# Kernel optimization log

Hardware: AMD Instinct MI355X
Metric: run time of the kernel (lower is better)

## Reference

```python
import jax, jax.numpy as jnp
import numpy as np

N = 50000
E = 800000
IN_DIM = 128
HID = 64
HEADS = 4
OUT = 64


def _bn(x, g, b, eps=1e-5):
    # BatchNorm1d with batch statistics (biased var), as in train-mode normalization
    mu = x.mean(0)
    var = ((x - mu) ** 2).mean(0)
    return (x - mu) * jax.lax.rsqrt(var + eps) * g + b


def _gat(x, W, a_src, a_dst, bias, src, dst, heads, dim, concat):
    # PyG GATConv: h = xW; e_ij = LeakyReLU(a_src.h_j + a_dst.h_i); softmax over incoming edges of i
    n = x.shape[0]
    h = (x @ W).reshape(n, heads, dim)            # [N,H,D]
    es = (h * a_src).sum(-1)                      # [N,H]
    ed = (h * a_dst).sum(-1)                      # [N,H]
    e = jax.nn.leaky_relu(es[src] + ed[dst], 0.2)  # [E,H]
    emax = jax.ops.segment_max(e, dst, num_segments=n)
    w = jnp.exp(e - emax[dst])
    denom = jax.ops.segment_sum(w, dst, num_segments=n)
    alpha = w / (denom[dst] + 1e-16)              # [E,H]
    out = jax.ops.segment_sum(h[src] * alpha[:, :, None], dst, num_segments=n)  # [N,H,D]
    out = out.reshape(n, heads * dim) if concat else out.mean(axis=1)
    return out + bias


def _gcn(x, W, bias, src, dst):
    # PyG GCNConv with self-loops (already appended): D^{-1/2} A D^{-1/2} x W
    n = x.shape[0]
    h = x @ W
    deg = jax.ops.segment_sum(jnp.ones(src.shape[0], h.dtype), dst, num_segments=n)
    dinv = jax.lax.rsqrt(jnp.maximum(deg, 1e-12))
    norm = dinv[src] * dinv[dst]                  # [E]
    return jax.ops.segment_sum(h[src] * norm[:, None], dst, num_segments=n) + bias


def setup_inputs() -> dict:
    key = jax.random.key(0)
    ks = jax.random.split(key, 16)
    s = 0.1
    inp = {
        "x": jax.random.normal(ks[0], (N, IN_DIM), jnp.float32),
        "edge_index": jax.random.randint(ks[1], (2, E), 0, N, jnp.int64 if jax.config.jax_enable_x64 else jnp.int32),
        "edge_attr": jax.random.normal(ks[2], (E,), jnp.float32),
        # GAT layer 1
        "W1": jax.random.normal(ks[3], (IN_DIM, HEADS * HID), jnp.float32) * s,
        "att_src1": jax.random.normal(ks[4], (HEADS, HID), jnp.float32) * s,
        "att_dst1": jax.random.normal(ks[5], (HEADS, HID), jnp.float32) * s,
        "b1": jnp.zeros((HEADS * HID,), jnp.float32),
        "g1": jnp.ones((HEADS * HID,), jnp.float32),
        "beta1": jnp.zeros((HEADS * HID,), jnp.float32),
        # GCN
        "Wg": jax.random.normal(ks[6], (HEADS * HID, HID), jnp.float32) * s,
        "bg": jnp.zeros((HID,), jnp.float32),
        "g2": jnp.ones((HID,), jnp.float32),
        "beta2": jnp.zeros((HID,), jnp.float32),
        # GAT layer 2 (heads=1, concat=False)
        "W2": jax.random.normal(ks[7], (HID, OUT), jnp.float32) * s,
        "att_src2": jax.random.normal(ks[8], (1, OUT), jnp.float32) * s,
        "att_dst2": jax.random.normal(ks[9], (1, OUT), jnp.float32) * s,
        "b2": jnp.zeros((OUT,), jnp.float32),
        "g3": jnp.ones((OUT,), jnp.float32),
        "beta3": jnp.zeros((OUT,), jnp.float32),
        # projector
        "Wp1": jax.random.normal(ks[10], (OUT, 128), jnp.float32) * s,
        "bp1": jnp.zeros((128,), jnp.float32),
        "Wp2": jax.random.normal(ks[11], (128, 64), jnp.float32) * s,
        "bp2": jnp.zeros((64,), jnp.float32),
    }
    return inp


def reference(x, edge_index, edge_attr, W1, att_src1, att_dst1, b1, g1, beta1,
              Wg, bg, g2, beta2, W2, att_src2, att_dst2, b2, g3, beta3,
              Wp1, bp1, Wp2, bp2):
    # edge_attr is ignored by GATConv when edge_dim is None (PyG behavior)
    loop = jnp.arange(N, dtype=edge_index.dtype)
    src = jnp.concatenate([edge_index[0], loop])  # self-loops appended
    dst = jnp.concatenate([edge_index[1], loop])
    h = _gat(x, W1, att_src1, att_dst1, b1, src, dst, HEADS, HID, True)
    h = jax.nn.elu(_bn(h, g1, beta1))
    h = _gcn(h, Wg, bg, src, dst)
    h = jax.nn.relu(_bn(h, g2, beta2))
    h = _gat(h, W2, att_src2, att_dst2, b2, src, dst, 1, OUT, False)
    h = jax.nn.elu(_bn(h, g3, beta3))
    return jax.nn.relu(h @ Wp1 + bp1) @ Wp2 + bp2
```

## Files before the change

kernel.cpp:

```cpp
#include <hip/hip_runtime.h>
#include <math.h>

#define NN 50000
#define EE 800000
#define E2 850000
#define SCB 196
#define GXL 391

typedef __attribute__((ext_vector_type(8))) short short8;
typedef __attribute__((ext_vector_type(8))) unsigned short ushort8v;
typedef __attribute__((ext_vector_type(4))) float float4v;

__device__ __forceinline__ float bf2f(unsigned short u) {
  return __uint_as_float(((unsigned int)u) << 16);
}
__device__ __forceinline__ unsigned short f2bf(float f) {
  unsigned int x = __float_as_uint(f);
  unsigned int r = (x + 0x7fffu + ((x >> 16) & 1u)) >> 16;
  return (unsigned short)r;
}

__device__ __forceinline__ float leaky(float x) { return x > 0.f ? x : 0.2f * x; }

__device__ __forceinline__ int edge_src(const int* ei, int e) {
  return (e < EE) ? ei[e] : (e - EE);
}
__device__ __forceinline__ int edge_dst(const int* ei, int e) {
  return (e < EE) ? ei[EE + e] : (e - EE);
}

__global__ void k_deg(const int* __restrict__ ei, int* __restrict__ deg) {
  int e = blockIdx.x * blockDim.x + threadIdx.x;
  if (e < E2) atomicAdd(&deg[edge_dst(ei, e)], 1);
}

__global__ __launch_bounds__(256) void k_scan1(const int* __restrict__ deg,
                                               int* __restrict__ partial) {
  __shared__ int sd[256];
  int i = blockIdx.x * 256 + threadIdx.x;
  sd[threadIdx.x] = (i < NN) ? deg[i] : 0;
  __syncthreads();
  for (int off = 128; off > 0; off >>= 1) {
    if (threadIdx.x < off) sd[threadIdx.x] += sd[threadIdx.x + off];
    __syncthreads();
  }
  if (threadIdx.x == 0) partial[blockIdx.x] = sd[0];
}

__global__ __launch_bounds__(256) void k_scan3(const int* __restrict__ deg,
                                               const int* __restrict__ partial,
                                               int* __restrict__ rowptr,
                                               int* __restrict__ cnt,
                                               float* __restrict__ dinv) {
  __shared__ int sp[256];
  __shared__ int sd[256];
  int t = threadIdx.x;
  sp[t] = (t < SCB) ? partial[t] : 0;
  __syncthreads();
  for (int off = 1; off < 256; off <<= 1) {
    int v = (t >= off) ? sp[t - off] : 0;
    __syncthreads();
    sp[t] += v;
    __syncthreads();
  }
  int base = (blockIdx.x == 0) ? 0 : sp[blockIdx.x - 1];
  int i = blockIdx.x * 256 + t;
  int v = (i < NN) ? deg[i] : 0;
  sd[t] = v;
  __syncthreads();
  for (int off = 1; off < 256; off <<= 1) {
    int u = (t >= off) ? sd[t - off] : 0;
    __syncthreads();
    sd[t] += u;
    __syncthreads();
  }
  if (i < NN) {
    int excl = base + sd[t] - v;
    rowptr[i] = excl;
    cnt[i] = excl;
    dinv[i] = rsqrtf((float)v);
  }
  if (i == 0) rowptr[NN] = E2;
}

__global__ void k_fill(const int* __restrict__ ei, int* __restrict__ cnt,
                       int* __restrict__ csr) {
  int e = blockIdx.x * blockDim.x + threadIdx.x;
  if (e >= E2) return;
  int d = edge_dst(ei, e);
  int s = edge_src(ei, e);
  int pos = atomicAdd(&cnt[d], 1);
  csr[pos] = s;
}

__global__ __launch_bounds__(256) void k_gemm1(
    const float* __restrict__ A, const float* __restrict__ B,
    unsigned short* __restrict__ Cbf,
    const float* __restrict__ attSrc, const float* __restrict__ attDst,
    float* __restrict__ esOut, float* __restrict__ edOut, int M) {
  __shared__ unsigned short BT[64][136];
  int t = threadIdx.x;
  int lane = t & 63;
  int wv = t >> 6;
  int cl = lane & 15;
  int kg = lane >> 4;
  int rowBase = blockIdx.x * 128;

  short8 afr[2][4];
  int grA0 = rowBase + wv * 32 + cl;
#pragma unroll
  for (int rt = 0; rt < 2; ++rt) {
    int gr = grA0 + rt * 16;
#pragma unroll
    for (int ks = 0; ks < 4; ++ks) {
      int k0 = ks * 32 + kg * 8;
      if (gr < M) {
        float4 f0 = *(const float4*)&A[(size_t)gr * 128 + k0];
        float4 f1 = *(const float4*)&A[(size_t)gr * 128 + k0 + 4];
        afr[rt][ks][0] = (short)f2bf(f0.x); afr[rt][ks][1] = (short)f2bf(f0.y);
        afr[rt][ks][2] = (short)f2bf(f0.z); afr[rt][ks][3] = (short)f2bf(f0.w);
        afr[rt][ks][4] = (short)f2bf(f1.x); afr[rt][ks][5] = (short)f2bf(f1.y);
        afr[rt][ks][6] = (short)f2bf(f1.z); afr[rt][ks][7] = (short)f2bf(f1.w);
      } else {
#pragma unroll
        for (int j = 0; j < 8; ++j) afr[rt][ks][j] = 0;
      }
    }
  }

  for (int cg = 0; cg < 4; ++cg) {
    int colBase = cg * 64;
    {
      int c = t & 63;
      for (int k = t >> 6; k < 128; k += 4)
        BT[c][k] = f2bf(B[(size_t)k * 256 + colBase + c]);
    }
    __syncthreads();

    float4v acc[2][4];
#pragma unroll
    for (int rt = 0; rt < 2; ++rt)
#pragma unroll
      for (int ct = 0; ct < 4; ++ct) acc[rt][ct] = (float4v){0.f, 0.f, 0.f, 0.f};

#pragma unroll
    for (int ks = 0; ks < 4; ++ks) {
      int k0 = ks * 32 + kg * 8;
      short8 bfr[4];
#pragma unroll
      for (int ct = 0; ct < 4; ++ct)
        bfr[ct] = *(const short8*)&BT[ct * 16 + cl][k0];
#pragma unroll
      for (int rt = 0; rt < 2; ++rt)
#pragma unroll
        for (int ct = 0; ct < 4; ++ct)
          acc[rt][ct] = __builtin_amdgcn_mfma_f32_16x16x32_bf16(
              afr[rt][ks], bfr[ct], acc[rt][ct], 0, 0, 0);
    }

    float as4[4], ad4[4];
#pragma unroll
    for (int ct = 0; ct < 4; ++ct) {
      int gc = colBase + ct * 16 + cl;
      as4[ct] = attSrc[gc];
      ad4[ct] = attDst[gc];
    }
#pragma unroll
    for (int rt = 0; rt < 2; ++rt) {
      float pes[4] = {0.f, 0.f, 0.f, 0.f};
      float ped[4] = {0.f, 0.f, 0.f, 0.f};
#pragma unroll
      for (int reg = 0; reg < 4; ++reg) {
        int gr = rowBase + wv * 32 + rt * 16 + kg * 4 + reg;
        bool ok = gr < M;
#pragma unroll
        for (int ct = 0; ct < 4; ++ct) {
          float v = acc[rt][ct][reg];
          int gc = colBase + ct * 16 + cl;
          if (ok) Cbf[(size_t)gr * 256 + gc] = f2bf(v);
          pes[reg] = fmaf(v, as4[ct], pes[reg]);
          ped[reg] = fmaf(v, ad4[ct], ped[reg]);
        }
      }
#pragma unroll
      for (int reg = 0; reg < 4; ++reg) {
#pragma unroll
        for (int off = 8; off > 0; off >>= 1) {
          pes[reg] += __shfl_xor(pes[reg], off);
          ped[reg] += __shfl_xor(ped[reg], off);
        }
      }
      if (cl == 0) {
#pragma unroll
        for (int reg = 0; reg < 4; ++reg) {
          int gr = rowBase + wv * 32 + rt * 16 + kg * 4 + reg;
          if (gr < M) {
            esOut[gr * 4 + cg] = pes[reg];
            edOut[gr * 4 + cg] = ped[reg];
          }
        }
      }
    }
    __syncthreads();
  }
}

template <int K, int ATTMODE, int INACT, bool ABF, bool USEBN>
__global__ __launch_bounds__(256) void k_gemm_mfma(
    const float* __restrict__ A, const unsigned short* __restrict__ Abf,
    const float* __restrict__ B, const float* __restrict__ biasOut,
    const float* __restrict__ bnst, const float* __restrict__ bng,
    const float* __restrict__ bnb, int outAct,
    float* __restrict__ Cf, unsigned short* __restrict__ Cbf,
    const float* __restrict__ rowScale,
    const float* __restrict__ attSrc, const float* __restrict__ attDst,
    float* __restrict__ esOut, float* __restrict__ edOut,
    int M, int NC) {
  __shared__ unsigned short BT[64][K + 8];
  __shared__ float sSc[256], sSh[256];
  int t = threadIdx.x;
  int lane = t & 63;
  int wv = t >> 6;
  int cl = lane & 15;
  int kg = lane >> 4;
  int rowBase = blockIdx.x * 128;
  int colBase = blockIdx.y * 64;

  if (USEBN) {
    int c = t;
    if (c < K) {
      float sum = 0.f, sq = 0.f;
      for (int cp = 0; cp < 32; ++cp) {
        sum += bnst[cp * 2 * K + c];
        sq += bnst[cp * 2 * K + K + c];
      }
      const float invN = 1.0f / (float)NN;
      float mu = sum * invN;
      float var = sq * invN - mu * mu;
      float rs = rsqrtf(var + 1e-5f);
      float sc = rs * bng[c];
      sSc[c] = sc;
      sSh[c] = fmaf(-mu, sc, bnb[c]);
    }
  }
  {
    int c = t & 63;
    for (int k = t >> 6; k < K; k += 4)
      BT[c][k] = f2bf(B[(size_t)k * NC + colBase + c]);
  }
  __syncthreads();

  float4v acc[2][4];
#pragma unroll
  for (int rt = 0; rt < 2; ++rt)
#pragma unroll
    for (int ct = 0; ct < 4; ++ct) acc[rt][ct] = (float4v){0.f, 0.f, 0.f, 0.f};

  int grA0 = rowBase + wv * 32 + cl;
  int grA1 = grA0 + 16;

#pragma unroll
  for (int kc = 0; kc < K; kc += 32) {
    int k0 = kc + kg * 8;
    short8 afr[2];
#pragma unroll
    for (int rt = 0; rt < 2; ++rt) {
      int gr = rt ? grA1 : grA0;
      float v[8];
      if (gr < M) {
        if (ABF) {
          ushort4 u0 = *(const ushort4*)&Abf[(size_t)gr * K + k0];
          ushort4 u1 = *(const ushort4*)&Abf[(size_t)gr * K + k0 + 4];
          v[0] = bf2f(u0.x); v[1] = bf2f(u0.y); v[2] = bf2f(u0.z); v[3] = bf2f(u0.w);
          v[4] = bf2f(u1.x); v[5] = bf2f(u1.y); v[6] = bf2f(u1.z); v[7] = bf2f(u1.w);
        } else {
          float4 f0 = *(const float4*)&A[(size_t)gr * K + k0];
          float4 f1 = *(const float4*)&A[(size_t)gr * K + k0 + 4];
          v[0] = f0.x; v[1] = f0.y; v[2] = f0.z; v[3] = f0.w;
          v[4] = f1.x; v[5] = f1.y; v[6] = f1.z; v[7] = f1.w;
        }
      } else {
#pragma unroll
        for (int i = 0; i < 8; ++i) v[i] = 0.f;
      }
#pragma unroll
      for (int i = 0; i < 8; ++i) {
        float x = v[i];
        if (USEBN) x = fmaf(x, sSc[k0 + i], sSh[k0 + i]);
        if (INACT == 1) x = fmaxf(x, 0.f);
        else if (INACT == 2) x = (x > 0.f) ? x : expm1f(x);
        afr[rt][i] = (short)f2bf(x);
      }
    }
    short8 bfr[4];
#pragma unroll
    for (int ct = 0; ct < 4; ++ct)
      bfr[ct] = *(const short8*)&BT[ct * 16 + cl][k0];
#pragma unroll
    for (int rt = 0; rt < 2; ++rt)
#pragma unroll
      for (int ct = 0; ct < 4; ++ct)
        acc[rt][ct] = __builtin_amdgcn_mfma_f32_16x16x32_bf16(
            afr[rt], bfr[ct], acc[rt][ct], 0, 0, 0);
  }

  float bb[4], as4[4], ad4[4];
#pragma unroll
  for (int ct = 0; ct < 4; ++ct) {
    int gc = colBase + ct * 16 + cl;
    bb[ct] = biasOut ? biasOut[gc] : 0.f;
    if (ATTMODE) {
      as4[ct] = attSrc[gc];
      ad4[ct] = attDst[gc];
    }
  }
#pragma unroll
  for (int rt = 0; rt < 2; ++rt) {
    float pes[4] = {0.f, 0.f, 0.f, 0.f};
    float ped[4] = {0.f, 0.f, 0.f, 0.f};
#pragma unroll
    for (int reg = 0; reg < 4; ++reg) {
      int gr = rowBase + wv * 32 + rt * 16 + kg * 4 + reg;
      bool ok = gr < M;
      float rs_ = 1.f;
      if (ok && Cbf && rowScale) rs_ = rowScale[gr];
#pragma unroll
      for (int ct = 0; ct < 4; ++ct) {
        float v = acc[rt][ct][reg] + bb[ct];
        if (outAct == 1) v = fmaxf(v, 0.f);
        int gc = colBase + ct * 16 + cl;
        if (ok) {
          if (Cf) Cf[(size_t)gr * NC + gc] = v;
          if (Cbf) Cbf[(size_t)gr * NC + gc] = f2bf(v * rs_);
        }
        if (ATTMODE) {
          pes[reg] = fmaf(v, as4[ct], pes[reg]);
          ped[reg] = fmaf(v, ad4[ct], ped[reg]);
        }
      }
    }
    if (ATTMODE) {
#pragma unroll
      for (int reg = 0; reg < 4; ++reg) {
#pragma unroll
        for (int off = 8; off > 0; off >>= 1) {
          pes[reg] += __shfl_xor(pes[reg], off);
          ped[reg] += __shfl_xor(ped[reg], off);
        }
      }
      if (cl == 0) {
#pragma unroll
        for (int reg = 0; reg < 4; ++reg) {
          int gr = rowBase + wv * 32 + rt * 16 + kg * 4 + reg;
          if (gr < M) {
            if (ATTMODE == 1) {
              esOut[gr * 4 + blockIdx.y] = pes[reg];
              edOut[gr * 4 + blockIdx.y] = ped[reg];
            } else {
              esOut[gr] = pes[reg];
              edOut[gr] = ped[reg];
            }
          }
        }
      }
    }
  }
}

__global__ __launch_bounds__(256) void k_soft1(const float* __restrict__ es,
                                               const float* __restrict__ ed,
                                               const int* __restrict__ rowptr,
                                               const int* __restrict__ csr,
                                               float* __restrict__ w1) {
  int node = blockIdx.x * 16 + (threadIdx.x >> 4);
  int sub = threadIdx.x & 15;
  int start = rowptr[node], end = rowptr[node + 1];
  float4 edv = *(const float4*)&ed[node * 4];
  float m0 = -1e30f, m1 = -1e30f, m2 = -1e30f, m3 = -1e30f;
  float s0 = 0.f, s1 = 0.f, s2 = 0.f, s3 = 0.f;
  for (int k = start + sub; k < end; k += 16) {
    int s = csr[k];
    float4 esv = *(const float4*)&es[s * 4];
    float e0 = leaky(esv.x + edv.x);
    float e1 = leaky(esv.y + edv.y);
    float e2 = leaky(esv.z + edv.z);
    float e3 = leaky(esv.w + edv.w);
    float mn;
    mn = fmaxf(m0, e0); s0 = s0 * __expf(m0 - mn) + __expf(e0 - mn); m0 = mn;
    mn = fmaxf(m1, e1); s1 = s1 * __expf(m1 - mn) + __expf(e1 - mn); m1 = mn;
    mn = fmaxf(m2, e2); s2 = s2 * __expf(m2 - mn) + __expf(e2 - mn); m2 = mn;
    mn = fmaxf(m3, e3); s3 = s3 * __expf(m3 - mn) + __expf(e3 - mn); m3 = mn;
  }
#pragma unroll
  for (int off = 1; off < 16; off <<= 1) {
    float mo, so, mn;
    mo = __shfl_xor(m0, off); so = __shfl_xor(s0, off);
    mn = fmaxf(m0, mo); s0 = s0 * __expf(m0 - mn) + so * __expf(mo - mn); m0 = mn;
    mo = __shfl_xor(m1, off); so = __shfl_xor(s1, off);
    mn = fmaxf(m1, mo); s1 = s1 * __expf(m1 - mn) + so * __expf(mo - mn); m1 = mn;
    mo = __shfl_xor(m2, off); so = __shfl_xor(s2, off);
    mn = fmaxf(m2, mo); s2 = s2 * __expf(m2 - mn) + so * __expf(mo - mn); m2 = mn;
    mo = __shfl_xor(m3, off); so = __shfl_xor(s3, off);
    mn = fmaxf(m3, mo); s3 = s3 * __expf(m3 - mn) + so * __expf(mo - mn); m3 = mn;
  }
  float i0 = 1.f / (s0 + 1e-16f);
  float i1 = 1.f / (s1 + 1e-16f);
  float i2 = 1.f / (s2 + 1e-16f);
  float i3 = 1.f / (s3 + 1e-16f);
  for (int k = start + sub; k < end; k += 16) {
    int s = csr[k];
    float4 esv = *(const float4*)&es[s * 4];
    w1[k]          = __expf(leaky(esv.x + edv.x) - m0) * i0;
    w1[E2 + k]     = __expf(leaky(esv.y + edv.y) - m1) * i1;
    w1[2 * E2 + k] = __expf(leaky(esv.z + edv.z) - m2) * i2;
    w1[3 * E2 + k] = __expf(leaky(esv.w + edv.w) - m3) * i3;
  }
}

__global__ __launch_bounds__(256) void k_soft2(const float* __restrict__ es,
                                               const float* __restrict__ ed,
                                               const int* __restrict__ rowptr,
                                               const int* __restrict__ csr,
                                               float* __restrict__ w2) {
  int node = blockIdx.x * 16 + (threadIdx.x >> 4);
  int sub = threadIdx.x & 15;
  int start = rowptr[node], end = rowptr[node + 1];
  float edi = ed[node];
  float m = -1e30f, ss = 0.f;
  for (int k = start + sub; k < end; k += 16) {
    float e = leaky(es[csr[k]] + edi);
    float mn = fmaxf(m, e);
    ss = ss * __expf(m - mn) + __expf(e - mn);
    m = mn;
  }
#pragma unroll
  for (int off = 1; off < 16; off <<= 1) {
    float mo = __shfl_xor(m, off);
    float so = __shfl_xor(ss, off);
    float mn = fmaxf(m, mo);
    ss = ss * __expf(m - mn) + so * __expf(mo - mn);
    m = mn;
  }
  float inv = 1.f / (ss + 1e-16f);
  for (int k = start + sub; k < end; k += 16) {
    float e = leaky(es[csr[k]] + edi);
    w2[k] = __expf(e - m) * inv;
  }
}

__global__ __launch_bounds__(256) void k_gat1(const unsigned short* __restrict__ h1b,
                                              const float* __restrict__ w1,
                                              const int* __restrict__ rowptr,
                                              const int* __restrict__ csr,
                                              const float* __restrict__ b1,
                                              unsigned short* __restrict__ outb,
                                              float* __restrict__ st) {
  __shared__ float smS[4][256];
  __shared__ float smQ[4][256];
  int wave = threadIdx.x >> 6;
  int lane = threadIdx.x & 63;
  int i = blockIdx.x * 4 + wave;
  int start = rowptr[i], end = rowptr[i + 1];
  int half = lane >> 5;
  int cl5 = lane & 31;
  int head = cl5 >> 3;
  int cOff = cl5 * 8;
  const float* wh = w1 + (size_t)head * E2;
  float acc[8];
#pragma unroll
  for (int j = 0; j < 8; ++j) acc[j] = 0.f;

  int k = start;
  for (; k + 4 <= end; k += 4) {
#pragma unroll
    for (int u = 0; u < 2; ++u) {
      int kk = k + u * 2 + half;
      int s = csr[kk];
      float wv = wh[kk];
      ushort8v hv = *(const ushort8v*)&h1b[(size_t)s * 256 + cOff];
#pragma unroll
      for (int j = 0; j < 8; ++j) acc[j] = fmaf(bf2f(hv[j]), wv, acc[j]);
    }
  }
  for (; k + 2 <= end; k += 2) {
    int kk = k + half;
    int s = csr[kk];
    float wv = wh[kk];
    ushort8v hv = *(const ushort8v*)&h1b[(size_t)s * 256 + cOff];
#pragma unroll
    for (int j = 0; j < 8; ++j) acc[j] = fmaf(bf2f(hv[j]), wv, acc[j]);
  }
  if (k < end) {
    int s = csr[k];
    float wv = (half == 0) ? wh[k] : 0.f;
    ushort8v hv = *(const ushort8v*)&h1b[(size_t)s * 256 + cOff];
#pragma unroll
    for (int j = 0; j < 8; ++j) acc[j] = fmaf(bf2f(hv[j]), wv, acc[j]);
  }
#pragma unroll
  for (int j = 0; j < 8; ++j) acc[j] += __shfl_xor(acc[j], 32);

  float4 b0 = *(const float4*)&b1[cOff];
  float4 b1v = *(const float4*)&b1[cOff + 4];
  float bb[8] = {b0.x, b0.y, b0.z, b0.w, b1v.x, b1v.y, b1v.z, b1v.w};
  if (half == 0) {
    float o[8];
    ushort8v u8;
#pragma unroll
    for (int j = 0; j < 8; ++j) {
      o[j] = acc[j] + bb[j];
      u8[j] = f2bf(o[j]);
    }
    *(ushort8v*)&outb[(size_t)i * 256 + cOff] = u8;
    float4 s0 = make_float4(o[0], o[1], o[2], o[3]);
    float4 s1 = make_float4(o[4], o[5], o[6], o[7]);
    *(float4*)&smS[wave][cOff] = s0;
    *(float4*)&smS[wave][cOff + 4] = s1;
    float4 q0 = make_float4(o[0]*o[0], o[1]*o[1], o[2]*o[2], o[3]*o[3]);
    float4 q1 = make_float4(o[4]*o[4], o[5]*o[5], o[6]*o[6], o[7]*o[7]);
    *(float4*)&smQ[wave][cOff] = q0;
    *(float4*)&smQ[wave][cOff + 4] = q1;
  }
  __syncthreads();
  int c = threadIdx.x;
  float s_ = 0.f, q_ = 0.f;
#pragma unroll
  for (int wv = 0; wv < 4; ++wv) { s_ += smS[wv][c]; q_ += smQ[wv][c]; }
  float* dst = st + (size_t)(blockIdx.x & 31) * 512;
  atomicAdd(&dst[c], s_);
  atomicAdd(&dst[256 + c], q_);
}

__global__ __launch_bounds__(256) void k_gcn(const unsigned short* __restrict__ hgb,
                                             const float* __restrict__ dinv,
                                             const int* __restrict__ rowptr,
                                             const int* __restrict__ csr,
                                             const float* __restrict__ bg,
                                             unsigned short* __restrict__ outb,
                                             float* __restrict__ st) {
  __shared__ float smS[4][64];
  __shared__ float smQ[4][64];
  int wave = threadIdx.x >> 6;
  int lane = threadIdx.x & 63;
  int i = blockIdx.x * 4 + wave;
  int start = rowptr[i], end = rowptr[i + 1];
  int grp = lane >> 3;
  int cOff = (lane & 7) * 8;
  float acc[8];
#pragma unroll
  for (int j = 0; j < 8; ++j) acc[j] = 0.f;

  int k = start;
  for (; k + 8 <= end; k += 8) {
    int s = csr[k + grp];
    ushort8v hv = *(const ushort8v*)&hgb[(size_t)s * 64 + cOff];
#pragma unroll
    for (int j = 0; j < 8; ++j) acc[j] += bf2f(hv[j]);
  }
  if (k < end) {
    int kk = k + grp;
    bool act = kk < end;
    int s = csr[act ? kk : start];
    float m_ = act ? 1.f : 0.f;
    ushort8v hv = *(const ushort8v*)&hgb[(size_t)s * 64 + cOff];
#pragma unroll
    for (int j = 0; j < 8; ++j) acc[j] = fmaf(bf2f(hv[j]), m_, acc[j]);
  }
#pragma unroll
  for (int off = 8; off <= 32; off <<= 1)
#pragma unroll
    for (int j = 0; j < 8; ++j) acc[j] += __shfl_xor(acc[j], off);

  if (lane < 8) {
    float di = dinv[i];
    float4 g0 = *(const float4*)&bg[cOff];
    float4 g1 = *(const float4*)&bg[cOff + 4];
    float bb[8] = {g0.x, g0.y, g0.z, g0.w, g1.x, g1.y, g1.z, g1.w};
    float o[8];
    ushort8v u8;
#pragma unroll
    for (int j = 0; j < 8; ++j) {
      o[j] = fmaf(acc[j], di, bb[j]);
      u8[j] = f2bf(o[j]);
      smS[wave][cOff + j] = o[j];
      smQ[wave][cOff + j] = o[j] * o[j];
    }
    *(ushort8v*)&outb[(size_t)i * 64 + cOff] = u8;
  }
  __syncthreads();
  if (threadIdx.x < 64) {
    int c = threadIdx.x;
    float s_ = 0.f, q_ = 0.f;
#pragma unroll
    for (int wv = 0; wv < 4; ++wv) { s_ += smS[wv][c]; q_ += smQ[wv][c]; }
    float* dst = st + (size_t)(blockIdx.x & 31) * 128;
    atomicAdd(&dst[c], s_);
    atomicAdd(&dst[64 + c], q_);
  }
}

__global__ __launch_bounds__(256) void k_gat2(const unsigned short* __restrict__ h2b,
                                              const float* __restrict__ w2,
                                              const int* __restrict__ rowptr,
                                              const int* __restrict__ csr,
                                              const float* __restrict__ b2,
                                              unsigned short* __restrict__ outb,
                                              float* __restrict__ st) {
  __shared__ float smS[4][64];
  __shared__ float smQ[4][64];
  int wave = threadIdx.x >> 6;
  int lane = threadIdx.x & 63;
  int i = blockIdx.x * 4 + wave;
  int start = rowptr[i], end = rowptr[i + 1];
  int grp = lane >> 3;
  int cOff = (lane & 7) * 8;
  float acc[8];
#pragma unroll
  for (int j = 0; j < 8; ++j) acc[j] = 0.f;

  int k = start;
  for (; k + 8 <= end; k += 8) {
    int kk = k + grp;
    int s = csr[kk];
    float wv = w2[kk];
    ushort8v hv = *(const ushort8v*)&h2b[(size_t)s * 64 + cOff];
#pragma unroll
    for (int j = 0; j < 8; ++j) acc[j] = fmaf(bf2f(hv[j]), wv, acc[j]);
  }
  if (k < end) {
    int kk = k + grp;
    bool act = kk < end;
    int s = csr[act ? kk : start];
    float wv = act ? w2[kk] : 0.f;
    ushort8v hv = *(const ushort8v*)&h2b[(size_t)s * 64 + cOff];
#pragma unroll
    for (int j = 0; j < 8; ++j) acc[j] = fmaf(bf2f(hv[j]), wv, acc[j]);
  }
#pragma unroll
  for (int off = 8; off <= 32; off <<= 1)
#pragma unroll
    for (int j = 0; j < 8; ++j) acc[j] += __shfl_xor(acc[j], off);

  if (lane < 8) {
    float4 g0 = *(const float4*)&b2[cOff];
    float4 g1 = *(const float4*)&b2[cOff + 4];
    float bb[8] = {g0.x, g0.y, g0.z, g0.w, g1.x, g1.y, g1.z, g1.w};
    float o[8];
    ushort8v u8;
#pragma unroll
    for (int j = 0; j < 8; ++j) {
      o[j] = acc[j] + bb[j];
      u8[j] = f2bf(o[j]);
      smS[wave][cOff + j] = o[j];
      smQ[wave][cOff + j] = o[j] * o[j];
    }
    *(ushort8v*)&outb[(size_t)i * 64 + cOff] = u8;
  }
  __syncthreads();
  if (threadIdx.x < 64) {
    int c = threadIdx.x;
    float s_ = 0.f, q_ = 0.f;
#pragma unroll
    for (int wv = 0; wv < 4; ++wv) { s_ += smS[wv][c]; q_ += smQ[wv][c]; }
    float* dst = st + (size_t)(blockIdx.x & 31) * 128;
    atomicAdd(&dst[c], s_);
    atomicAdd(&dst[64 + c], q_);
  }
}

extern "C" void kernel_launch(void* const* d_in, const int* in_sizes, int n_in,
                              void* d_out, int out_size, void* d_ws, size_t ws_size,
                              hipStream_t stream) {
  const float* x        = (const float*)d_in[0];
  const int*   ei       = (const int*)d_in[1];
  const float* W1       = (const float*)d_in[3];
  const float* att_src1 = (const float*)d_in[4];
  const float* att_dst1 = (const float*)d_in[5];
  const float* b1       = (const float*)d_in[6];
  const float* g1       = (const float*)d_in[7];
  const float* beta1    = (const float*)d_in[8];
  const float* Wg       = (const float*)d_in[9];
  const float* bg       = (const float*)d_in[10];
  const float* g2       = (const float*)d_in[11];
  const float* beta2    = (const float*)d_in[12];
  const float* W2       = (const float*)d_in[13];
  const float* att_src2 = (const float*)d_in[14];
  const float* att_dst2 = (const float*)d_in[15];
  const float* b2       = (const float*)d_in[16];
  const float* g3       = (const float*)d_in[17];
  const float* beta3    = (const float*)d_in[18];
  const float* Wp1      = (const float*)d_in[19];
  const float* bp1      = (const float*)d_in[20];
  const float* Wp2      = (const float*)d_in[21];
  const float* bp2      = (const float*)d_in[22];
  float* out = (float*)d_out;

  char* w = (char*)d_ws;
  unsigned short* bufBb  = (unsigned short*)(w + 0);
  unsigned short* bufDb  = (unsigned short*)(w + 0);
  unsigned short* h1b    = (unsigned short*)(w + 51200000);
  unsigned short* hiddenb= (unsigned short*)(w + 51200000);
  float*          w1     = (float*)(w + 76800000);
  float*          w2     = (float*)(w + 76800000);
  unsigned short* hgb    = (unsigned short*)(w + 90400000);
  unsigned short* bufCb  = (unsigned short*)(w + 96800000);
  unsigned short* h2b    = (unsigned short*)(w + 109600000);
  float*          es1    = (float*)(w + 116000000);
  float*          ed1    = (float*)(w + 116800000);
  float*          es2    = (float*)(w + 117600000);
  float*          ed2    = (float*)(w + 117800000);
  float*          dinv   = (float*)(w + 118000000);
  int*            deg    = (int*)(w + 118200000);
  int*            rowptr = (int*)(w + 118400000);
  int*            cnt    = (int*)(w + 118600064);
  int*            csr    = (int*)(w + 118800064);
  float*          st1    = (float*)(w + 122200064);
  float*          st2    = st1 + 32 * 512;
  float*          st3    = st2 + 32 * 128;
  int*            partial= (int*)(st3 + 32 * 128);

  hipMemsetAsync(deg, 0, NN * sizeof(int), stream);
  hipMemsetAsync(st1, 0, (32 * 512 + 32 * 128 + 32 * 128) * sizeof(float), stream);

  const int EB = (E2 + 255) / 256;
  const int WB = NN / 4;
  const int SB = NN / 16;

  k_deg<<<EB, 256, 0, stream>>>(ei, deg);
  k_scan1<<<SCB, 256, 0, stream>>>(deg, partial);
  k_scan3<<<SCB, 256, 0, stream>>>(deg, partial, rowptr, cnt, dinv);
  k_fill<<<EB, 256, 0, stream>>>(ei, cnt, csr);

  k_gemm1<<<GXL, 256, 0, stream>>>(x, W1, h1b, att_src1, att_dst1, es1, ed1, NN);
  k_soft1<<<SB, 256, 0, stream>>>(es1, ed1, rowptr, csr, w1);
  k_gat1<<<WB, 256, 0, stream>>>(h1b, w1, rowptr, csr, b1, bufBb, st1);

  k_gemm_mfma<256, 0, 2, true, true><<<dim3(GXL, 1), 256, 0, stream>>>(
      nullptr, bufBb, Wg, nullptr, st1, g1, beta1, 0,
      nullptr, hgb, dinv, nullptr, nullptr, nullptr, nullptr, NN, 64);
  k_gcn<<<WB, 256, 0, stream>>>(hgb, dinv, rowptr, csr, bg, bufCb, st2);

  k_gemm_mfma<64, 2, 1, true, true><<<dim3(GXL, 1), 256, 0, stream>>>(
      nullptr, bufCb, W2, nullptr, st2, g2, beta2, 0,
      nullptr, h2b, nullptr, att_src2, att_dst2, es2, ed2, NN, 64);
  k_soft2<<<SB, 256, 0, stream>>>(es2, ed2, rowptr, csr, w2);
  k_gat2<<<WB, 256, 0, stream>>>(h2b, w2, rowptr, csr, b2, bufDb, st3);

  k_gemm_mfma<64, 0, 2, true, true><<<dim3(GXL, 2), 256, 0, stream>>>(
      nullptr, bufDb, Wp1, bp1, st3, g3, beta3, 1,
      nullptr, hiddenb, nullptr, nullptr, nullptr, nullptr, nullptr, NN, 128);
  k_gemm_mfma<128, 0, 0, true, false><<<dim3(GXL, 1), 256, 0, stream>>>(
      nullptr, hiddenb, Wp2, bp2, nullptr, nullptr, nullptr, 0,
      out, nullptr, nullptr, nullptr, nullptr, nullptr, nullptr, NN, 64);
}
```

Measured before the change: 450.0 us.

## Fuse edge softmax into GAT aggregation kernels, dropping the attention weight buffers

Removes the separate k_soft1/k_soft2 kernels. Each GAT aggregation wave now computes the per-node online max and sum over incoming edges itself, then recomputes the normalized attention weight inline from es/ed while gathering neighbor features. This avoids writing and re-reading the E x 4 (and E x 1) float weight arrays and saves two launches. In exchange, es is gathered twice per edge and the exponentials are evaluated redundantly across the lanes that share a head.

```diff
diff --git a/kernel.cpp b/kernel.cpp
--- a/kernel.cpp
+++ b/kernel.cpp
@@ -367,18 +367,25 @@
   }
 }
 
-__global__ __launch_bounds__(256) void k_soft1(const float* __restrict__ es,
-                                               const float* __restrict__ ed,
-                                               const int* __restrict__ rowptr,
-                                               const int* __restrict__ csr,
-                                               float* __restrict__ w1) {
-  int node = blockIdx.x * 16 + (threadIdx.x >> 4);
-  int sub = threadIdx.x & 15;
-  int start = rowptr[node], end = rowptr[node + 1];
-  float4 edv = *(const float4*)&ed[node * 4];
+__global__ __launch_bounds__(256) void k_gat1(const unsigned short* __restrict__ h1b,
+                                              const float* __restrict__ es,
+                                              const float* __restrict__ ed,
+                                              const int* __restrict__ rowptr,
+                                              const int* __restrict__ csr,
+                                              const float* __restrict__ b1,
+                                              unsigned short* __restrict__ outb,
+                                              float* __restrict__ st) {
+  __shared__ float smS[4][256];
+  __shared__ float smQ[4][256];
+  int wave = threadIdx.x >> 6;
+  int lane = threadIdx.x & 63;
+  int i = blockIdx.x * 4 + wave;
+  int start = rowptr[i], end = rowptr[i + 1];
+  float4 edv = *(const float4*)&ed[i * 4];
+
   float m0 = -1e30f, m1 = -1e30f, m2 = -1e30f, m3 = -1e30f;
   float s0 = 0.f, s1 = 0.f, s2 = 0.f, s3 = 0.f;
-  for (int k = start + sub; k < end; k += 16) {
+  for (int k = start + lane; k < end; k += 64) {
     int s = csr[k];
     float4 esv = *(const float4*)&es[s * 4];
     float e0 = leaky(esv.x + edv.x);
@@ -392,7 +399,7 @@
     mn = fmaxf(m3, e3); s3 = s3 * __expf(m3 - mn) + __expf(e3 - mn); m3 = mn;
   }
 #pragma unroll
-  for (int off = 1; off < 16; off <<= 1) {
+  for (int off = 1; off < 64; off <<= 1) {
     float mo, so, mn;
     mo = __shfl_xor(m0, off); so = __shfl_xor(s0, off);
     mn = fmaxf(m0, mo); s0 = s0 * __expf(m0 - mn) + so * __expf(mo - mn); m0 = mn;
@@ -403,69 +410,16 @@
     mo = __shfl_xor(m3, off); so = __shfl_xor(s3, off);
     mn = fmaxf(m3, mo); s3 = s3 * __expf(m3 - mn) + so * __expf(mo - mn); m3 = mn;
   }
-  float i0 = 1.f / (s0 + 1e-16f);
-  float i1 = 1.f / (s1 + 1e-16f);
-  float i2 = 1.f / (s2 + 1e-16f);
-  float i3 = 1.f / (s3 + 1e-16f);
-  for (int k = start + sub; k < end; k += 16) {
-    int s = csr[k];
-    float4 esv = *(const float4*)&es[s * 4];
-    w1[k]          = __expf(leaky(esv.x + edv.x) - m0) * i0;
-    w1[E2 + k]     = __expf(leaky(esv.y + edv.y) - m1) * i1;
-    w1[2 * E2 + k] = __expf(leaky(esv.z + edv.z) - m2) * i2;
-    w1[3 * E2 + k] = __expf(leaky(esv.w + edv.w) - m3) * i3;
-  }
-}
-
-__global__ __launch_bounds__(256) void k_soft2(const float* __restrict__ es,
-                                               const float* __restrict__ ed,
-                                               const int* __restrict__ rowptr,
-                                               const int* __restrict__ csr,
-                                               float* __restrict__ w2) {
-  int node = blockIdx.x * 16 + (threadIdx.x >> 4);
-  int sub = threadIdx.x & 15;
-  int start = rowptr[node], end = rowptr[node + 1];
-  float edi = ed[node];
-  float m = -1e30f, ss = 0.f;
-  for (int k = start + sub; k < end; k += 16) {
-    float e = leaky(es[csr[k]] + edi);
-    float mn = fmaxf(m, e);
-    ss = ss * __expf(m - mn) + __expf(e - mn);
-    m = mn;
-  }
-#pragma unroll
-  for (int off = 1; off < 16; off <<= 1) {
-    float mo = __shfl_xor(m, off);
-    float so = __shfl_xor(ss, off);
-    float mn = fmaxf(m, mo);
-    ss = ss * __expf(m - mn) + so * __expf(mo - mn);
-    m = mn;
-  }
-  float inv = 1.f / (ss + 1e-16f);
-  for (int k = start + sub; k < end; k += 16) {
-    float e = leaky(es[csr[k]] + edi);
-    w2[k] = __expf(e - m) * inv;
-  }
-}
-
-__global__ __launch_bounds__(256) void k_gat1(const unsigned short* __restrict__ h1b,
-                                              const float* __restrict__ w1,
-                                              const int* __restrict__ rowptr,
-                                              const int* __restrict__ csr,
-                                              const float* __restrict__ b1,
-                                              unsigned short* __restrict__ outb,
-                                              float* __restrict__ st) {
-  __shared__ float smS[4][256];
-  __shared__ float smQ[4][256];
-  int wave = threadIdx.x >> 6;
-  int lane = threadIdx.x & 63;
-  int i = blockIdx.x * 4 + wave;
-  int start = rowptr[i], end = rowptr[i + 1];
+
   int half = lane >> 5;
   int cl5 = lane & 31;
   int head = cl5 >> 3;
   int cOff = cl5 * 8;
-  const float* wh = w1 + (size_t)head * E2;
+  float mh  = (head == 0) ? m0 : (head == 1) ? m1 : (head == 2) ? m2 : m3;
+  float sh  = (head == 0) ? s0 : (head == 1) ? s1 : (head == 2) ? s2 : s3;
+  float edh = (head == 0) ? edv.x : (head == 1) ? edv.y : (head == 2) ? edv.z : edv.w;
+  float inv = 1.f / (sh + 1e-16f);
+
   float acc[8];
 #pragma unroll
   for (int j = 0; j < 8; ++j) acc[j] = 0.f;
@@ -476,7 +430,8 @@
     for (int u = 0; u < 2; ++u) {
       int kk = k + u * 2 + half;
       int s = csr[kk];
-      float wv = wh[kk];
+      float e = leaky(es[s * 4 + head] + edh);
+      float wv = __expf(e - mh) * inv;
       ushort8v hv = *(const ushort8v*)&h1b[(size_t)s * 256 + cOff];
 #pragma unroll
       for (int j = 0; j < 8; ++j) acc[j] = fmaf(bf2f(hv[j]), wv, acc[j]);
@@ -485,14 +440,16 @@
   for (; k + 2 <= end; k += 2) {
     int kk = k + half;
     int s = csr[kk];
-    float wv = wh[kk];
+    float e = leaky(es[s * 4 + head] + edh);
+    float wv = __expf(e - mh) * inv;
     ushort8v hv = *(const ushort8v*)&h1b[(size_t)s * 256 + cOff];
 #pragma unroll
     for (int j = 0; j < 8; ++j) acc[j] = fmaf(bf2f(hv[j]), wv, acc[j]);
   }
   if (k < end) {
     int s = csr[k];
-    float wv = (half == 0) ? wh[k] : 0.f;
+    float e = leaky(es[s * 4 + head] + edh);
+    float wv = (half == 0) ? __expf(e - mh) * inv : 0.f;
     ushort8v hv = *(const ushort8v*)&h1b[(size_t)s * 256 + cOff];
 #pragma unroll
     for (int j = 0; j < 8; ++j) acc[j] = fmaf(bf2f(hv[j]), wv, acc[j]);
@@ -512,10 +469,10 @@
       u8[j] = f2bf(o[j]);
     }
     *(ushort8v*)&outb[(size_t)i * 256 + cOff] = u8;
-    float4 s0 = make_float4(o[0], o[1], o[2], o[3]);
-    float4 s1 = make_float4(o[4], o[5], o[6], o[7]);
-    *(float4*)&smS[wave][cOff] = s0;
-    *(float4*)&smS[wave][cOff + 4] = s1;
+    float4 s0_ = make_float4(o[0], o[1], o[2], o[3]);
+    float4 s1_ = make_float4(o[4], o[5], o[6], o[7]);
+    *(float4*)&smS[wave][cOff] = s0_;
+    *(float4*)&smS[wave][cOff + 4] = s1_;
     float4 q0 = make_float4(o[0]*o[0], o[1]*o[1], o[2]*o[2], o[3]*o[3]);
     float4 q1 = make_float4(o[4]*o[4], o[5]*o[5], o[6]*o[6], o[7]*o[7]);
     *(float4*)&smQ[wave][cOff] = q0;
@@ -600,7 +557,8 @@
 }
 
 __global__ __launch_bounds__(256) void k_gat2(const unsigned short* __restrict__ h2b,
-                                              const float* __restrict__ w2,
+                                              const float* __restrict__ es,
+                                              const float* __restrict__ ed,
                                               const int* __restrict__ rowptr,
                                               const int* __restrict__ csr,
                                               const float* __restrict__ b2,
@@ -612,6 +570,25 @@
   int lane = threadIdx.x & 63;
   int i = blockIdx.x * 4 + wave;
   int start = rowptr[i], end = rowptr[i + 1];
+  float edi = ed[i];
+
+  float m = -1e30f, ss = 0.f;
+  for (int k = start + lane; k < end; k += 64) {
+    float e = leaky(es[csr[k]] + edi);
+    float mn = fmaxf(m, e);
+    ss = ss * __expf(m - mn) + __expf(e - mn);
+    m = mn;
+  }
+#pragma unroll
+  for (int off = 1; off < 64; off <<= 1) {
+    float mo = __shfl_xor(m, off);
+    float so = __shfl_xor(ss, off);
+    float mn = fmaxf(m, mo);
+    ss = ss * __expf(m - mn) + so * __expf(mo - mn);
+    m = mn;
+  }
+  float inv = 1.f / (ss + 1e-16f);
+
   int grp = lane >> 3;
   int cOff = (lane & 7) * 8;
   float acc[8];
@@ -622,7 +599,8 @@
   for (; k + 8 <= end; k += 8) {
     int kk = k + grp;
     int s = csr[kk];
-    float wv = w2[kk];
+    float e = leaky(es[s] + edi);
+    float wv = __expf(e - m) * inv;
     ushort8v hv = *(const ushort8v*)&h2b[(size_t)s * 64 + cOff];
 #pragma unroll
     for (int j = 0; j < 8; ++j) acc[j] = fmaf(bf2f(hv[j]), wv, acc[j]);
@@ -631,7 +609,8 @@
     int kk = k + grp;
     bool act = kk < end;
     int s = csr[act ? kk : start];
-    float wv = act ? w2[kk] : 0.f;
+    float e = leaky(es[s] + edi);
+    float wv = act ? __expf(e - m) * inv : 0.f;
     ushort8v hv = *(const ushort8v*)&h2b[(size_t)s * 64 + cOff];
 #pragma unroll
     for (int j = 0; j < 8; ++j) acc[j] = fmaf(bf2f(hv[j]), wv, acc[j]);
@@ -700,8 +679,6 @@
   unsigned short* bufDb  = (unsigned short*)(w + 0);
   unsigned short* h1b    = (unsigned short*)(w + 51200000);
   unsigned short* hiddenb= (unsigned short*)(w + 51200000);
-  float*          w1     = (float*)(w + 76800000);
-  float*          w2     = (float*)(w + 76800000);
   unsigned short* hgb    = (unsigned short*)(w + 90400000);
   unsigned short* bufCb  = (unsigned short*)(w + 96800000);
   unsigned short* h2b    = (unsigned short*)(w + 109600000);
@@ -724,7 +701,6 @@
 
   const int EB = (E2 + 255) / 256;
   const int WB = NN / 4;
-  const int SB = NN / 16;
 
   k_deg<<<EB, 256, 0, stream>>>(ei, deg);
   k_scan1<<<SCB, 256, 0, stream>>>(deg, partial);
@@ -732,8 +708,7 @@
   k_fill<<<EB, 256, 0, stream>>>(ei, cnt, csr);
 
   k_gemm1<<<GXL, 256, 0, stream>>>(x, W1, h1b, att_src1, att_dst1, es1, ed1, NN);
-  k_soft1<<<SB, 256, 0, stream>>>(es1, ed1, rowptr, csr, w1);
-  k_gat1<<<WB, 256, 0, stream>>>(h1b, w1, rowptr, csr, b1, bufBb, st1);
+  k_gat1<<<WB, 256, 0, stream>>>(h1b, es1, ed1, rowptr, csr, b1, bufBb, st1);
 
   k_gemm_mfma<256, 0, 2, true, true><<<dim3(GXL, 1), 256, 0, stream>>>(
       nullptr, bufBb, Wg, nullptr, st1, g1, beta1, 0,
@@ -743,8 +718,7 @@
   k_gemm_mfma<64, 2, 1, true, true><<<dim3(GXL, 1), 256, 0, stream>>>(
       nullptr, bufCb, W2, nullptr, st2, g2, beta2, 0,
       nullptr, h2b, nullptr, att_src2, att_dst2, es2, ed2, NN, 64);
-  k_soft2<<<SB, 256, 0, stream>>>(es2, ed2, rowptr, csr, w2);
-  k_gat2<<<WB, 256, 0, stream>>>(h2b, w2, rowptr, csr, b2, bufDb, st3);
+  k_gat2<<<WB, 256, 0, stream>>>(h2b, es2, ed2, rowptr, csr, b2, bufDb, st3);
 
   k_gemm_mfma<64, 0, 2, true, true><<<dim3(GXL, 2), 256, 0, stream>>>(
       nullptr, bufDb, Wp1, bp1, st3, g3, beta3, 1,
```

After: 439.2 us. -2.4%, faster.
